# Optimization experiments

Measured on AMD Instinct MI355X. Metric: run time of the kernel, lower is better.

Reference implementation:

```python
import jax, jax.numpy as jnp
import numpy as np

KERNEL = (3, 3, 3)
STRIDE = (1, 1, 1)
PAD = (1, 1, 1)
DIL = (1, 1, 1)


def setup_inputs() -> dict:
    key = jax.random.key(0)
    k1, k2 = jax.random.split(key)
    # input: [B, C, D, H, W]
    x = jax.random.normal(k1, (2, 64, 16, 64, 64), dtype=jnp.float32)
    # per-pixel weights: [B, heads, weight_channels, kernel_volume, D_out, H_out, W_out]
    weight = jax.random.normal(k2, (2, 1, 16, 27, 16, 64, 64), dtype=jnp.float32)
    return {"x": x, "weight": weight}


def _aggregate(x, weight):
    # involution-style 3D local aggregation with zero padding.
    B, C, D, H, W = x.shape
    _, heads, wc, kvol, Do, Ho, Wo = weight.shape
    kd, kh, kw = KERNEL
    assert kvol == kd * kh * kw and C % wc == 0
    Q = C // wc  # channel-sharing groups: channel c uses weight channel c % wc
    xp = jnp.pad(x, ((0, 0), (0, 0), (PAD[0], PAD[0]), (PAD[1], PAD[1]), (PAD[2], PAD[2])))
    # channels laid out so that c = q*wc + r -> weight channel r == c % wc
    out = jnp.zeros((B, heads, Q, wc, Do, Ho, Wo), dtype=x.dtype)
    for ikd in range(kd):
        for ikh in range(kh):
            for ikw in range(kw):  # fixed small structural loop (27 taps)
                k = (ikd * kh + ikh) * kw + ikw
                d0 = ikd * DIL[0]
                h0 = ikh * DIL[1]
                w0 = ikw * DIL[2]
                x_k = xp[:, :,
                         d0:d0 + (Do - 1) * STRIDE[0] + 1:STRIDE[0],
                         h0:h0 + (Ho - 1) * STRIDE[1] + 1:STRIDE[1],
                         w0:w0 + (Wo - 1) * STRIDE[2] + 1:STRIDE[2]]
                x_k = x_k.reshape(B, Q, wc, Do, Ho, Wo)
                # [B,1,Q,wc,Do,Ho,Wo] * [B,heads,1,wc,Do,Ho,Wo]
                out = out + x_k[:, None] * weight[:, :, None, :, k]
    return out.reshape(B, heads * C, Do, Ho, Wo)


def reference(x, weight):
    return _aggregate(x, weight)
```

## Files before the change

### kernel.cpp

```cpp
#include <hip/hip_runtime.h>
#include <stdint.h>


#define NQ 4
typedef float f4_t __attribute__((ext_vector_type(4)));

#define BUF_FLOATS (NQ * 18 * 64)
#define LDS_FLOATS (16 + 2 * BUF_FLOATS + 16)

__device__ __forceinline__ void async_copy16(const float* gsrc, float* ldst) {
    __builtin_amdgcn_global_load_lds(
        (const __attribute__((address_space(1))) uint32_t*)gsrc,
        (__attribute__((address_space(3))) uint32_t*)ldst, 16, 0, 0);
}

__global__ __launch_bounds__(256) void lconv_kernel(
    const float* __restrict__ x, const float* __restrict__ wt, float* __restrict__ out,
    const float* __restrict__ zp)
{
    __shared__ __align__(16) float lds_raw[LDS_FLOATS];

    const int tid = threadIdx.x;
    const int tw  = tid & 15;
    const int th  = tid >> 4;

    const int bid  = blockIdx.x;
    const int slot = bid >> 3;
    const int bc   = (bid & 7) * 4 + (slot >> 6);
    const int dout = (slot >> 2) & 15;
    const int ho_tile = slot & 3;
    const int b = bc >> 4, c = bc & 15;

    const int ho_base = ho_tile * 16;
    const int ho  = ho_base + th;
    const int wo0 = tw * 4;

    const float* xbase = x + ((size_t)(b * 64 + c) * 16) * 4096;

    auto stage = [&](int buf, int d) {
        float* dbase = &lds_raw[16 + buf * BUF_FLOATS];
        #pragma unroll
        for (int it = 0; it < 5; ++it) {
            const int i = it * 256 + tid;
            if (it < 4 || i < 1152) {
                const int row = i >> 4;
                const int seg = i & 15;
                const int q   = row / 18;
                const int hl  = row - q * 18;
                const int gh  = ho_base - 1 + hl;
                const float* src = ((unsigned)gh < 64u)
                    ? (xbase + (size_t)q * 1048576 + (size_t)d * 4096
                             + (size_t)gh * 64 + seg * 4)
                    : (zp + seg * 4);
                async_copy16(src, dbase + (size_t)i * 4);
            }
        }
    };

    float acc[NQ][4];
    #pragma unroll
    for (int q = 0; q < NQ; ++q)
        #pragma unroll
        for (int j = 0; j < 4; ++j) acc[q][j] = 0.f;

    const float* wbase = wt + (((size_t)(b * 16 + c) * 27) * 16 + dout) * 4096
                            + (size_t)ho * 64 + wo0;

    if (dout > 0) stage(0, dout - 1);
    __syncthreads();

    #pragma unroll
    for (int dd = 0; dd < 3; ++dd) {
        const int cur = dd & 1, nxt = cur ^ 1;
        if (dd < 2 && dout + dd < 16) stage(nxt, dout + dd);

        const int d = dout + dd - 1;
        if ((unsigned)d < 16u) {
            const float* bbase = &lds_raw[16 + cur * BUF_FLOATS];
            #pragma unroll
            for (int dh = 0; dh < 3; ++dh) {
                float xv[NQ][6];
                #pragma unroll
                for (int q = 0; q < NQ; ++q) {
                    const float* r = bbase + (q * 18 + th + dh) * 64;
                    const f4_t m = *reinterpret_cast<const f4_t*>(r + wo0);
                    const float xl = r[wo0 - 1];
                    const float xr = r[wo0 + 4];
                    xv[q][0] = (tw > 0)  ? xl : 0.f;
                    xv[q][1] = m.x; xv[q][2] = m.y; xv[q][3] = m.z; xv[q][4] = m.w;
                    xv[q][5] = (tw < 15) ? xr : 0.f;
                }
                #pragma unroll
                for (int dw = 0; dw < 3; ++dw) {
                    const int k = (dd * 3 + dh) * 3 + dw;
                    const f4_t w4 = __builtin_nontemporal_load(
                        reinterpret_cast<const f4_t*>(wbase + (size_t)k * 65536));
                    #pragma unroll
                    for (int q = 0; q < NQ; ++q) {
                        acc[q][0] = fmaf(xv[q][0 + dw], w4.x, acc[q][0]);
                        acc[q][1] = fmaf(xv[q][1 + dw], w4.y, acc[q][1]);
                        acc[q][2] = fmaf(xv[q][2 + dw], w4.z, acc[q][2]);
                        acc[q][3] = fmaf(xv[q][3 + dw], w4.w, acc[q][3]);
                    }
                }
            }
        }
        if (dd < 2) __syncthreads();
    }

    #pragma unroll
    for (int q = 0; q < NQ; ++q) {
        float* orow = out + ((size_t)(b * 64 + q * 16 + c) * 16 + dout) * 4096
                          + (size_t)ho * 64 + wo0;
        f4_t rr; rr.x = acc[q][0]; rr.y = acc[q][1]; rr.z = acc[q][2]; rr.w = acc[q][3];
        __builtin_nontemporal_store(rr, reinterpret_cast<f4_t*>(orow));
    }
}

extern "C" void kernel_launch(void* const* d_in, const int* in_sizes, int n_in,
                              void* d_out, int out_size, void* d_ws, size_t ws_size,
                              hipStream_t stream) {
    const float* x  = (const float*)d_in[0];
    const float* wt = (const float*)d_in[1];
    float* out      = (float*)d_out;

    hipMemsetAsync(d_ws, 0, 4096, stream);

    dim3 grid(2048), block(256);
    hipLaunchKernelGGL(lconv_kernel, grid, block, 0, stream, x, wt, out,
                       (const float*)d_ws);
}
```

Measured before the change: 56.40 us.

## Compute two output depth slices per block sharing four staged input planes

Each block now has 512 threads split into two teams that compute adjacent output depth slices. All four needed input depth planes are staged into LDS up front with a single barrier, replacing the per-depth double-buffered staging and its barriers. This cuts redundant input loads from three-fold to two-fold per depth and removes mid-loop syncs. In exchange it doubles LDS use and loses overlap between staging and compute, which may reduce occupancy.

```diff
diff --git a/kernel.cpp b/kernel.cpp
--- a/kernel.cpp
+++ b/kernel.cpp
@@ -6,7 +6,7 @@
 typedef float f4_t __attribute__((ext_vector_type(4)));
 
 #define BUF_FLOATS (NQ * 18 * 64)
-#define LDS_FLOATS (16 + 2 * BUF_FLOATS + 16)
+#define LDS_FLOATS (16 + 4 * BUF_FLOATS + 16)
 
 __device__ __forceinline__ void async_copy16(const float* gsrc, float* ldst) {
     __builtin_amdgcn_global_load_lds(
@@ -14,48 +14,56 @@
         (__attribute__((address_space(3))) uint32_t*)ldst, 16, 0, 0);
 }
 
-__global__ __launch_bounds__(256) void lconv_kernel(
+__global__ __launch_bounds__(512, 4) void lconv_kernel(
     const float* __restrict__ x, const float* __restrict__ wt, float* __restrict__ out,
     const float* __restrict__ zp)
 {
     __shared__ __align__(16) float lds_raw[LDS_FLOATS];
 
-    const int tid = threadIdx.x;
-    const int tw  = tid & 15;
-    const int th  = tid >> 4;
+    const int tid  = threadIdx.x;
+    const int team = tid >> 8;
+    const int t    = tid & 255;
+    const int tw   = t & 15;
+    const int th   = t >> 4;
 
-    const int bid  = blockIdx.x;
-    const int slot = bid >> 3;
-    const int bc   = (bid & 7) * 4 + (slot >> 6);
-    const int dout = (slot >> 2) & 15;
+    const int bid   = blockIdx.x;
+    const int slot  = bid >> 3;
+    const int bc    = (bid & 7) * 4 + (slot >> 5);
+    const int apair = (slot >> 2) & 7;
     const int ho_tile = slot & 3;
     const int b = bc >> 4, c = bc & 15;
 
     const int ho_base = ho_tile * 16;
     const int ho  = ho_base + th;
     const int wo0 = tw * 4;
+    const int d0  = apair * 2;
 
     const float* xbase = x + ((size_t)(b * 64 + c) * 16) * 4096;
 
-    auto stage = [&](int buf, int d) {
-        float* dbase = &lds_raw[16 + buf * BUF_FLOATS];
-        #pragma unroll
-        for (int it = 0; it < 5; ++it) {
-            const int i = it * 256 + tid;
-            if (it < 4 || i < 1152) {
-                const int row = i >> 4;
-                const int seg = i & 15;
-                const int q   = row / 18;
-                const int hl  = row - q * 18;
-                const int gh  = ho_base - 1 + hl;
-                const float* src = ((unsigned)gh < 64u)
-                    ? (xbase + (size_t)q * 1048576 + (size_t)d * 4096
-                             + (size_t)gh * 64 + seg * 4)
-                    : (zp + seg * 4);
-                async_copy16(src, dbase + (size_t)i * 4);
-            }
-        }
-    };
+    #pragma unroll
+    for (int it = 0; it < 9; ++it) {
+        const int i   = it * 512 + tid;
+        const int p   = i / 1152;
+        const int r2  = i - p * 1152;
+        const int row = r2 >> 4;
+        const int seg = r2 & 15;
+        const int q   = row / 18;
+        const int hl  = row - q * 18;
+        const int gh  = ho_base - 1 + hl;
+        const int d   = d0 - 1 + p;
+        const bool ok = ((unsigned)d < 16u) && ((unsigned)gh < 64u);
+        const float* src = ok
+            ? (xbase + (size_t)q * 1048576 + (size_t)d * 4096 + (size_t)gh * 64 + seg * 4)
+            : (zp + seg * 4);
+        const int buf = (d + 1) & 3;
+        async_copy16(src, &lds_raw[16 + buf * BUF_FLOATS + r2 * 4]);
+    }
+    __syncthreads();
+
+    const int dout = d0 + team;
+
+    const float* wbase = wt + (((size_t)(b * 16 + c) * 27) * 16 + dout) * 4096
+                            + (size_t)ho * 64 + wo0;
 
     float acc[NQ][4];
     #pragma unroll
@@ -63,49 +71,37 @@
         #pragma unroll
         for (int j = 0; j < 4; ++j) acc[q][j] = 0.f;
 
-    const float* wbase = wt + (((size_t)(b * 16 + c) * 27) * 16 + dout) * 4096
-                            + (size_t)ho * 64 + wo0;
-
-    if (dout > 0) stage(0, dout - 1);
-    __syncthreads();
-
     #pragma unroll
     for (int dd = 0; dd < 3; ++dd) {
-        const int cur = dd & 1, nxt = cur ^ 1;
-        if (dd < 2 && dout + dd < 16) stage(nxt, dout + dd);
-
-        const int d = dout + dd - 1;
-        if ((unsigned)d < 16u) {
-            const float* bbase = &lds_raw[16 + cur * BUF_FLOATS];
+        const int buf = (dout + dd) & 3;
+        const float* bbase = &lds_raw[16 + buf * BUF_FLOATS];
+        #pragma unroll
+        for (int dh = 0; dh < 3; ++dh) {
+            float xv[NQ][6];
             #pragma unroll
-            for (int dh = 0; dh < 3; ++dh) {
-                float xv[NQ][6];
+            for (int q = 0; q < NQ; ++q) {
+                const float* r = bbase + (q * 18 + th + dh) * 64;
+                const f4_t m = *reinterpret_cast<const f4_t*>(r + wo0);
+                const float xl = r[wo0 - 1];
+                const float xr = r[wo0 + 4];
+                xv[q][0] = (tw > 0)  ? xl : 0.f;
+                xv[q][1] = m.x; xv[q][2] = m.y; xv[q][3] = m.z; xv[q][4] = m.w;
+                xv[q][5] = (tw < 15) ? xr : 0.f;
+            }
+            #pragma unroll
+            for (int dw = 0; dw < 3; ++dw) {
+                const int k = (dd * 3 + dh) * 3 + dw;
+                const f4_t w4 = __builtin_nontemporal_load(
+                    reinterpret_cast<const f4_t*>(wbase + (size_t)k * 65536));
                 #pragma unroll
                 for (int q = 0; q < NQ; ++q) {
-                    const float* r = bbase + (q * 18 + th + dh) * 64;
-                    const f4_t m = *reinterpret_cast<const f4_t*>(r + wo0);
-                    const float xl = r[wo0 - 1];
-                    const float xr = r[wo0 + 4];
-                    xv[q][0] = (tw > 0)  ? xl : 0.f;
-                    xv[q][1] = m.x; xv[q][2] = m.y; xv[q][3] = m.z; xv[q][4] = m.w;
-                    xv[q][5] = (tw < 15) ? xr : 0.f;
-                }
-                #pragma unroll
-                for (int dw = 0; dw < 3; ++dw) {
-                    const int k = (dd * 3 + dh) * 3 + dw;
-                    const f4_t w4 = __builtin_nontemporal_load(
-                        reinterpret_cast<const f4_t*>(wbase + (size_t)k * 65536));
-                    #pragma unroll
-                    for (int q = 0; q < NQ; ++q) {
-                        acc[q][0] = fmaf(xv[q][0 + dw], w4.x, acc[q][0]);
-                        acc[q][1] = fmaf(xv[q][1 + dw], w4.y, acc[q][1]);
-                        acc[q][2] = fmaf(xv[q][2 + dw], w4.z, acc[q][2]);
-                        acc[q][3] = fmaf(xv[q][3 + dw], w4.w, acc[q][3]);
-                    }
+                    acc[q][0] = fmaf(xv[q][0 + dw], w4.x, acc[q][0]);
+                    acc[q][1] = fmaf(xv[q][1 + dw], w4.y, acc[q][1]);
+                    acc[q][2] = fmaf(xv[q][2 + dw], w4.z, acc[q][2]);
+                    acc[q][3] = fmaf(xv[q][3 + dw], w4.w, acc[q][3]);
                 }
             }
         }
-        if (dd < 2) __syncthreads();
     }
 
     #pragma unroll
@@ -126,7 +122,7 @@
 
     hipMemsetAsync(d_ws, 0, 4096, stream);
 
-    dim3 grid(2048), block(256);
+    dim3 grid(1024), block(512);
     hipLaunchKernelGGL(lconv_kernel, grid, block, 0, stream, x, wt, out,
                        (const float*)d_ws);
 }
```

Measured after the change: 72.88 us. +29.2%, slower.

## Compute two output depth slices per block to reuse staged input planes

Applied to the files above, without the earlier changes.

Each block now produces two adjacent output depth slices instead of one. It stages four input depth planes rather than three for two outputs, so each plane's LDS load and fragment reads serve both accumulators. The grid is halved. Input staging traffic and LDS reads per output drop, in exchange for doubled accumulators and weight registers (higher register pressure, possibly lower occupancy) and fewer blocks.

```diff
diff --git a/kernel.cpp b/kernel.cpp
--- a/kernel.cpp
+++ b/kernel.cpp
@@ -24,16 +24,17 @@
     const int tw  = tid & 15;
     const int th  = tid >> 4;
 
-    const int bid  = blockIdx.x;
-    const int slot = bid >> 3;
-    const int bc   = (bid & 7) * 4 + (slot >> 6);
-    const int dout = (slot >> 2) & 15;
+    const int bid   = blockIdx.x;
+    const int slot  = bid >> 3;
+    const int bc    = (bid & 7) * 4 + (slot >> 5);
+    const int a     = (slot >> 2) & 7;
     const int ho_tile = slot & 3;
     const int b = bc >> 4, c = bc & 15;
 
     const int ho_base = ho_tile * 16;
     const int ho  = ho_base + th;
     const int wo0 = tw * 4;
+    const int dlo = a * 2, dhi = dlo + 1;
 
     const float* xbase = x + ((size_t)(b * 64 + c) * 16) * 4096;
 
@@ -48,7 +49,8 @@
                 const int q   = row / 18;
                 const int hl  = row - q * 18;
                 const int gh  = ho_base - 1 + hl;
-                const float* src = ((unsigned)gh < 64u)
+                const bool ok = ((unsigned)d < 16u) && ((unsigned)gh < 64u);
+                const float* src = ok
                     ? (xbase + (size_t)q * 1048576 + (size_t)d * 4096
                              + (size_t)gh * 64 + seg * 4)
                     : (zp + seg * 4);
@@ -57,63 +59,83 @@
         }
     };
 
-    float acc[NQ][4];
+    float accL[NQ][4], accH[NQ][4];
     #pragma unroll
     for (int q = 0; q < NQ; ++q)
         #pragma unroll
-        for (int j = 0; j < 4; ++j) acc[q][j] = 0.f;
+        for (int j = 0; j < 4; ++j) { accL[q][j] = 0.f; accH[q][j] = 0.f; }
 
-    const float* wbase = wt + (((size_t)(b * 16 + c) * 27) * 16 + dout) * 4096
-                            + (size_t)ho * 64 + wo0;
+    const float* wlo = wt + (((size_t)(b * 16 + c) * 27) * 16 + dlo) * 4096
+                          + (size_t)ho * 64 + wo0;
+    const float* whi = wlo + 4096;
 
-    if (dout > 0) stage(0, dout - 1);
+    stage(0, dlo - 1);
     __syncthreads();
 
     #pragma unroll
-    for (int dd = 0; dd < 3; ++dd) {
-        const int cur = dd & 1, nxt = cur ^ 1;
-        if (dd < 2 && dout + dd < 16) stage(nxt, dout + dd);
+    for (int s = 0; s < 4; ++s) {
+        const int cur = s & 1, nxt = cur ^ 1;
+        if (s < 3) stage(nxt, dlo + s);
 
-        const int d = dout + dd - 1;
-        if ((unsigned)d < 16u) {
-            const float* bbase = &lds_raw[16 + cur * BUF_FLOATS];
+        const bool loA = (s < 3);
+        const bool hiA = (s >= 1);
+        const float* bbase = &lds_raw[16 + cur * BUF_FLOATS];
+
+        #pragma unroll
+        for (int dh = 0; dh < 3; ++dh) {
+            f4_t wa[3], wb[3];
             #pragma unroll
-            for (int dh = 0; dh < 3; ++dh) {
-                float xv[NQ][6];
-                #pragma unroll
-                for (int q = 0; q < NQ; ++q) {
-                    const float* r = bbase + (q * 18 + th + dh) * 64;
-                    const f4_t m = *reinterpret_cast<const f4_t*>(r + wo0);
-                    const float xl = r[wo0 - 1];
-                    const float xr = r[wo0 + 4];
-                    xv[q][0] = (tw > 0)  ? xl : 0.f;
-                    xv[q][1] = m.x; xv[q][2] = m.y; xv[q][3] = m.z; xv[q][4] = m.w;
-                    xv[q][5] = (tw < 15) ? xr : 0.f;
+            for (int dw = 0; dw < 3; ++dw) {
+                if (loA) {
+                    const int k = (s * 3 + dh) * 3 + dw;
+                    wa[dw] = __builtin_nontemporal_load(
+                        reinterpret_cast<const f4_t*>(wlo + (size_t)k * 65536));
                 }
+                if (hiA) {
+                    const int k = ((s - 1) * 3 + dh) * 3 + dw;
+                    wb[dw] = __builtin_nontemporal_load(
+                        reinterpret_cast<const f4_t*>(whi + (size_t)k * 65536));
+                }
+            }
+            #pragma unroll
+            for (int q = 0; q < NQ; ++q) {
+                const float* r = bbase + (q * 18 + th + dh) * 64;
+                const f4_t m = *reinterpret_cast<const f4_t*>(r + wo0);
+                const float xl = r[wo0 - 1];
+                const float xr = r[wo0 + 4];
+                float xv[6];
+                xv[0] = (tw > 0)  ? xl : 0.f;
+                xv[1] = m.x; xv[2] = m.y; xv[3] = m.z; xv[4] = m.w;
+                xv[5] = (tw < 15) ? xr : 0.f;
                 #pragma unroll
                 for (int dw = 0; dw < 3; ++dw) {
-                    const int k = (dd * 3 + dh) * 3 + dw;
-                    const f4_t w4 = __builtin_nontemporal_load(
-                        reinterpret_cast<const f4_t*>(wbase + (size_t)k * 65536));
-                    #pragma unroll
-                    for (int q = 0; q < NQ; ++q) {
-                        acc[q][0] = fmaf(xv[q][0 + dw], w4.x, acc[q][0]);
-                        acc[q][1] = fmaf(xv[q][1 + dw], w4.y, acc[q][1]);
-                        acc[q][2] = fmaf(xv[q][2 + dw], w4.z, acc[q][2]);
-                        acc[q][3] = fmaf(xv[q][3 + dw], w4.w, acc[q][3]);
+                    if (loA) {
+                        accL[q][0] = fmaf(xv[0 + dw], wa[dw].x, accL[q][0]);
+                        accL[q][1] = fmaf(xv[1 + dw], wa[dw].y, accL[q][1]);
+                        accL[q][2] = fmaf(xv[2 + dw], wa[dw].z, accL[q][2]);
+                        accL[q][3] = fmaf(xv[3 + dw], wa[dw].w, accL[q][3]);
+                    }
+                    if (hiA) {
+                        accH[q][0] = fmaf(xv[0 + dw], wb[dw].x, accH[q][0]);
+                        accH[q][1] = fmaf(xv[1 + dw], wb[dw].y, accH[q][1]);
+                        accH[q][2] = fmaf(xv[2 + dw], wb[dw].z, accH[q][2]);
+                        accH[q][3] = fmaf(xv[3 + dw], wb[dw].w, accH[q][3]);
                     }
                 }
             }
         }
-        if (dd < 2) __syncthreads();
+        if (s < 3) __syncthreads();
     }
 
     #pragma unroll
     for (int q = 0; q < NQ; ++q) {
-        float* orow = out + ((size_t)(b * 64 + q * 16 + c) * 16 + dout) * 4096
-                          + (size_t)ho * 64 + wo0;
-        f4_t rr; rr.x = acc[q][0]; rr.y = acc[q][1]; rr.z = acc[q][2]; rr.w = acc[q][3];
-        __builtin_nontemporal_store(rr, reinterpret_cast<f4_t*>(orow));
+        float* orowL = out + ((size_t)(b * 64 + q * 16 + c) * 16 + dlo) * 4096
+                           + (size_t)ho * 64 + wo0;
+        f4_t rl; rl.x = accL[q][0]; rl.y = accL[q][1]; rl.z = accL[q][2]; rl.w = accL[q][3];
+        __builtin_nontemporal_store(rl, reinterpret_cast<f4_t*>(orowL));
+        float* orowH = orowL + 4096;
+        f4_t rh; rh.x = accH[q][0]; rh.y = accH[q][1]; rh.z = accH[q][2]; rh.w = accH[q][3];
+        __builtin_nontemporal_store(rh, reinterpret_cast<f4_t*>(orowH));
     }
 }
 
@@ -126,7 +148,7 @@
 
     hipMemsetAsync(d_ws, 0, 4096, stream);
 
-    dim3 grid(2048), block(256);
+    dim3 grid(1024), block(256);
     hipLaunchKernelGGL(lconv_kernel, grid, block, 0, stream, x, wt, out,
                        (const float*)d_ws);
 }
```

Result: slower. 69.13 us (+22.6%).

## Software-pipeline weight loads and stage zero planes for depth boundaries

Applied to the files above, without the earlier changes.

Restructures the 27-tap loop into 9 row groups and double-buffers the per-tap weight vectors in registers, loading the next group's three weights before computing the current one. Depth-boundary slices are now staged as zero rows from the zero buffer instead of being skipped by a branch, so every block does the same uniform work. This hides global-load latency on the weight stream, at the cost of more registers and wasted work on boundary depth slices.

```diff
diff --git a/kernel.cpp b/kernel.cpp
--- a/kernel.cpp
+++ b/kernel.cpp
@@ -48,7 +48,8 @@
                 const int q   = row / 18;
                 const int hl  = row - q * 18;
                 const int gh  = ho_base - 1 + hl;
-                const float* src = ((unsigned)gh < 64u)
+                const bool ok = ((unsigned)d < 16u) && ((unsigned)gh < 64u);
+                const float* src = ok
                     ? (xbase + (size_t)q * 1048576 + (size_t)d * 4096
                              + (size_t)gh * 64 + seg * 4)
                     : (zp + seg * 4);
@@ -66,46 +67,59 @@
     const float* wbase = wt + (((size_t)(b * 16 + c) * 27) * 16 + dout) * 4096
                             + (size_t)ho * 64 + wo0;
 
-    if (dout > 0) stage(0, dout - 1);
+    f4_t wreg[2][3];
+
+    stage(0, dout - 1);
+    #pragma unroll
+    for (int dw = 0; dw < 3; ++dw)
+        wreg[0][dw] = __builtin_nontemporal_load(
+            reinterpret_cast<const f4_t*>(wbase + (size_t)dw * 65536));
     __syncthreads();
 
     #pragma unroll
-    for (int dd = 0; dd < 3; ++dd) {
-        const int cur = dd & 1, nxt = cur ^ 1;
-        if (dd < 2 && dout + dd < 16) stage(nxt, dout + dd);
+    for (int g = 0; g < 9; ++g) {
+        const int dd  = g / 3;
+        const int dh  = g - dd * 3;
+        const int cur = dd & 1;
 
-        const int d = dout + dd - 1;
-        if ((unsigned)d < 16u) {
-            const float* bbase = &lds_raw[16 + cur * BUF_FLOATS];
+        if (dh == 0 && dd < 2) stage(cur ^ 1, dout + dd);
+
+        if (g < 8) {
             #pragma unroll
-            for (int dh = 0; dh < 3; ++dh) {
-                float xv[NQ][6];
-                #pragma unroll
-                for (int q = 0; q < NQ; ++q) {
-                    const float* r = bbase + (q * 18 + th + dh) * 64;
-                    const f4_t m = *reinterpret_cast<const f4_t*>(r + wo0);
-                    const float xl = r[wo0 - 1];
-                    const float xr = r[wo0 + 4];
-                    xv[q][0] = (tw > 0)  ? xl : 0.f;
-                    xv[q][1] = m.x; xv[q][2] = m.y; xv[q][3] = m.z; xv[q][4] = m.w;
-                    xv[q][5] = (tw < 15) ? xr : 0.f;
-                }
-                #pragma unroll
-                for (int dw = 0; dw < 3; ++dw) {
-                    const int k = (dd * 3 + dh) * 3 + dw;
-                    const f4_t w4 = __builtin_nontemporal_load(
-                        reinterpret_cast<const f4_t*>(wbase + (size_t)k * 65536));
-                    #pragma unroll
-                    for (int q = 0; q < NQ; ++q) {
-                        acc[q][0] = fmaf(xv[q][0 + dw], w4.x, acc[q][0]);
-                        acc[q][1] = fmaf(xv[q][1 + dw], w4.y, acc[q][1]);
-                        acc[q][2] = fmaf(xv[q][2 + dw], w4.z, acc[q][2]);
-                        acc[q][3] = fmaf(xv[q][3 + dw], w4.w, acc[q][3]);
-                    }
-                }
-            }
+            for (int dw = 0; dw < 3; ++dw)
+                wreg[(g + 1) & 1][dw] = __builtin_nontemporal_load(
+                    reinterpret_cast<const f4_t*>(wbase + (size_t)((g + 1) * 3 + dw) * 65536));
         }
-        if (dd < 2) __syncthreads();
+
+        const f4_t wa0 = wreg[g & 1][0];
+        const f4_t wa1 = wreg[g & 1][1];
+        const f4_t wa2 = wreg[g & 1][2];
+
+        const float* r0 = &lds_raw[16 + cur * BUF_FLOATS] + (th + dh) * 64;
+
+        #pragma unroll
+        for (int q = 0; q < NQ; ++q) {
+            const float* r = r0 + q * (18 * 64);
+            const f4_t m  = *reinterpret_cast<const f4_t*>(r + wo0);
+            const float xl = r[wo0 - 1];
+            const float xr = r[wo0 + 4];
+            const float x0 = (tw > 0)  ? xl : 0.f;
+            const float x5 = (tw < 15) ? xr : 0.f;
+            acc[q][0] = fmaf(x0,  wa0.x, acc[q][0]);
+            acc[q][1] = fmaf(m.x, wa0.y, acc[q][1]);
+            acc[q][2] = fmaf(m.y, wa0.z, acc[q][2]);
+            acc[q][3] = fmaf(m.z, wa0.w, acc[q][3]);
+            acc[q][0] = fmaf(m.x, wa1.x, acc[q][0]);
+            acc[q][1] = fmaf(m.y, wa1.y, acc[q][1]);
+            acc[q][2] = fmaf(m.z, wa1.z, acc[q][2]);
+            acc[q][3] = fmaf(m.w, wa1.w, acc[q][3]);
+            acc[q][0] = fmaf(m.y, wa2.x, acc[q][0]);
+            acc[q][1] = fmaf(m.z, wa2.y, acc[q][1]);
+            acc[q][2] = fmaf(m.w, wa2.z, acc[q][2]);
+            acc[q][3] = fmaf(x5,  wa2.w, acc[q][3]);
+        }
+
+        if (dh == 2 && dd < 2) __syncthreads();
     }
 
     #pragma unroll
```

After: 65.82 us. +16.7%, slower.
